# Performance work log

Hardware: AMD Instinct MI355X
Metric: run time of the kernel (lower is better)

The kernel has to match this reference:

```python
import jax, jax.numpy as jnp
import numpy as np
from jax import lax

N = 16384          # total nodes
NUM_GRAPHS = 256   # graphs in the batch
K = 50             # self.knn
NUM_BINS = 5       # num_edge_features
RDF_CUTOFF = 10.0  # Angstrom-scale cutoff for Gaussian RDF smearing
BIG = 1e10         # masked-distance sentinel (finite, jit-safe)


def setup_inputs() -> dict:
    key = jax.random.key(0)
    k1, k2 = jax.random.split(key)
    # 3D pharmacophore coordinates, ~Angstrom scale
    pos = jax.random.normal(k1, (N, 3), dtype=jnp.float32) * 3.0
    # sorted graph-id vector (PyG `batch`)
    batch = jnp.sort(jax.random.randint(k2, (N,), 0, NUM_GRAPHS, dtype=jnp.int64))
    return {"pos": pos, "batch": batch}


def reference(pos, batch):
    n = pos.shape[0]
    # --- brute-force KNN graph (T.KNNGraph, per-graph via batch mask) ---
    sq = jnp.sum(pos * pos, axis=-1)                         # [n]
    d2 = sq[:, None] + sq[None, :] - 2.0 * (pos @ pos.T)     # [n, n]
    same_graph = batch[:, None] == batch[None, :]
    valid = same_graph & ~jnp.eye(n, dtype=bool)             # no self-loops
    d2m = jnp.where(valid, d2, BIG)
    neg_d2, nbr_idx = lax.top_k(-d2m, K)                     # [n, K] nearest by distance
    # symmetric-superset edge list: j -> i (source_to_target flow)
    src = nbr_idx.reshape(-1)                                # [n*K]
    dst = jnp.repeat(jnp.arange(n), K)                       # [n*K]
    edge_index = jnp.stack([src, dst])                       # [2, n*K]
    # --- T.Distance(norm=False): raw Euclidean edge lengths ---
    dist = jnp.sqrt(jnp.maximum(-neg_d2, 1e-12)).reshape(-1)  # [n*K]
    # --- DistanceRDF(num_bins): Gaussian smearing of distances over bins ---
    centers = jnp.linspace(0.0, RDF_CUTOFF, NUM_BINS, dtype=pos.dtype)
    spacing = RDF_CUTOFF / (NUM_BINS - 1)
    gamma = 1.0 / (2.0 * spacing * spacing)
    rdf = jnp.exp(-gamma * (dist[:, None] - centers[None, :]) ** 2)  # [n*K, NUM_BINS]
    return edge_index, dist, rdf
```

## Files before the change

### kernel.cpp

```cpp
#include <hip/hip_runtime.h>
#include <math.h>

#define NTOT  16384
#define NGR   256
#define KNN   50
#define NBINS 5
#define BIGF  1e10f
#define MAXJ  3

__global__ void bounds_kernel(const int* __restrict__ batch, int* __restrict__ bounds)
{
    const int t = blockIdx.x * blockDim.x + threadIdx.x;
    if (t > NGR) return;
    int lo = 0, hi = NTOT;
    while (lo < hi) {
        const int mid = (lo + hi) >> 1;
        if (batch[mid] < t) lo = mid + 1; else hi = mid;
    }
    bounds[t] = lo;
}

__device__ __forceinline__ float bcast_lane(float v, int l)
{
    return __uint_as_float(__builtin_amdgcn_readlane(__float_as_uint(v), l));
}

template <int JJ>
__device__ __forceinline__ void rank_loop(const float (&d2r)[MAXJ], int (&rank)[MAXJ],
                                          int cnt, int lane)
{
    #pragma unroll
    for (int j2 = 0; j2 < JJ; ++j2) {
        const int base = j2 * 64;
        const int kmax = min(64, cnt - base);
        const float mine = d2r[j2];
        for (int l2 = 0; l2 < kmax; ++l2) {
            const float dk = bcast_lane(mine, l2);
            const int k = base + l2;
            #pragma unroll
            for (int j = 0; j < JJ; ++j) {
                const int c = j * 64 + lane;
                rank[j] += (dk < d2r[j]) || (dk == d2r[j] && k < c);
            }
        }
    }
}

__global__ __launch_bounds__(256)
void knn_main(const float* __restrict__ pos,
              const int*   __restrict__ batch,
              const int*   __restrict__ bounds,
              float*       __restrict__ out)
{
    const int wid  = (blockIdx.x << 2) + (threadIdx.x >> 6);
    const int lane = threadIdx.x & 63;
    const int i = wid;
    if (i >= NTOT) return;

    const int g     = batch[i];
    const int start = bounds[g];
    const int end   = bounds[g + 1];
    const int cnt   = end - start;
    const int J     = (cnt + 63) >> 6;

    const float xi = pos[(size_t)i * 3 + 0];
    const float yi = pos[(size_t)i * 3 + 1];
    const float zi = pos[(size_t)i * 3 + 2];
    const float sqi = xi * xi + yi * yi + zi * zi;

    float d2r[MAXJ];
    #pragma unroll
    for (int j = 0; j < MAXJ; ++j) d2r[j] = BIGF;

    #pragma unroll
    for (int j = 0; j < MAXJ; ++j) {
        const int c = j * 64 + lane;
        if (j < J && c < cnt) {
            const int idx = start + c;
            float d2 = BIGF;
            if (idx != i) {
                const float xj = pos[(size_t)idx * 3 + 0];
                const float yj = pos[(size_t)idx * 3 + 1];
                const float zj = pos[(size_t)idx * 3 + 2];
                const float sqj = xj * xj + yj * yj + zj * zj;
                const float dot = xi * xj + yi * yj + zi * zj;
                d2 = sqi + sqj - 2.0f * dot;
            }
            d2r[j] = d2;
        }
    }

    int rank[MAXJ] = {0, 0, 0};
    if      (J == 1) rank_loop<1>(d2r, rank, cnt, lane);
    else if (J == 2) rank_loop<2>(d2r, rank, cnt, lane);
    else             rank_loop<3>(d2r, rank, cnt, lane);

    float* __restrict__ srcO  = out;
    float* __restrict__ dstO  = out + (size_t)NTOT * KNN;
    float* __restrict__ distO = out + (size_t)2 * NTOT * KNN;
    float* __restrict__ rdfO  = out + (size_t)3 * NTOT * KNN;

    const float centers[NBINS] = {0.0f, 2.5f, 5.0f, 7.5f, 10.0f};
    const float gamma = 0.08f;
    const float fi = (float)i;

    #pragma unroll
    for (int j = 0; j < MAXJ; ++j) {
        const int c = j * 64 + lane;
        if (j < J && c < cnt && (start + c) != i) {
            const int r = rank[j];
            if (r < KNN) {
                const size_t e = (size_t)i * KNN + r;
                srcO[e]  = (float)(start + c);
                dstO[e]  = fi;
                const float d = sqrtf(fmaxf(d2r[j], 1e-12f));
                distO[e] = d;
                #pragma unroll
                for (int b = 0; b < NBINS; ++b) {
                    const float dd = d - centers[b];
                    rdfO[e * NBINS + b] = expf(-gamma * dd * dd);
                }
            }
        }
    }

    for (int r = (cnt - 1) + lane; r < KNN; r += 64) {
        const int m = r - (cnt - 1);
        int jj;
        if (m < start)       jj = m;
        else if (m == start) jj = i;
        else                 jj = end + (m - start - 1);
        const size_t e = (size_t)i * KNN + r;
        srcO[e]  = (float)jj;
        dstO[e]  = fi;
        const float d = sqrtf(BIGF);
        distO[e] = d;
        #pragma unroll
        for (int b = 0; b < NBINS; ++b) {
            const float dd = d - centers[b];
            rdfO[e * NBINS + b] = expf(-gamma * dd * dd);
        }
    }
}

extern "C" void kernel_launch(void* const* d_in, const int* in_sizes, int n_in,
                              void* d_out, int out_size, void* d_ws, size_t ws_size,
                              hipStream_t stream) {
    const float* pos   = (const float*)d_in[0];
    const int*   batch = (const int*)d_in[1];
    float*       out   = (float*)d_out;
    int*         bounds = (int*)d_ws;

    bounds_kernel<<<dim3(1), dim3(320), 0, stream>>>(batch, bounds);
    knn_main<<<dim3(NTOT / 4), dim3(256), 0, stream>>>(pos, batch, bounds, out);
}
```

Measured before the change: 90.68 us.

## Rank neighbors with packed 64-bit sortable keys and parallelize graph-bounds search

Packs each candidate's squared distance, transformed into an order-preserving integer, together with its index into one 64-bit key. Counting rank then needs a single unsigned compare per pair instead of a float compare plus tie-break, and the broadcast loop is unrolled by 8. The graph-bounds kernel now runs one thread per node and writes boundaries wherever the graph id changes, replacing a per-graph binary search. It also uses fast __expf, writes constant padding values for the underflowing far-distance case, and adds an occupancy hint. The key-transform edge cases and the hardcoded padding constants could affect exactness.

```diff
diff --git a/kernel.cpp b/kernel.cpp
--- a/kernel.cpp
+++ b/kernel.cpp
@@ -8,54 +8,53 @@
 #define BIGF  1e10f
 #define MAXJ  3
 
-__global__ void bounds_kernel(const int* __restrict__ batch, int* __restrict__ bounds)
+__global__ __launch_bounds__(256)
+void bounds_kernel(const int* __restrict__ batch, int* __restrict__ bounds)
 {
-    const int t = blockIdx.x * blockDim.x + threadIdx.x;
-    if (t > NGR) return;
-    int lo = 0, hi = NTOT;
-    while (lo < hi) {
-        const int mid = (lo + hi) >> 1;
-        if (batch[mid] < t) lo = mid + 1; else hi = mid;
-    }
-    bounds[t] = lo;
+    const int i = blockIdx.x * 256 + threadIdx.x;
+    if (i > NTOT) return;
+    const int cur  = (i < NTOT) ? batch[i] : NGR;
+    const int prev = (i == 0) ? -1 : batch[i - 1];
+    for (int t = prev + 1; t <= cur; ++t) bounds[t] = i;
 }
 
-__device__ __forceinline__ float bcast_lane(float v, int l)
+__device__ __forceinline__ unsigned int rdlane(unsigned int v, int l)
 {
-    return __uint_as_float(__builtin_amdgcn_readlane(__float_as_uint(v), l));
+    return (unsigned int)__builtin_amdgcn_readlane((int)v, l);
 }
 
-template <int JJ>
-__device__ __forceinline__ void rank_loop(const float (&d2r)[MAXJ], int (&rank)[MAXJ],
-                                          int cnt, int lane)
+template <int J>
+__device__ __forceinline__ void rank_count(const unsigned long long (&key)[MAXJ],
+                                           int (&rank)[MAXJ], int cnt)
 {
     #pragma unroll
-    for (int j2 = 0; j2 < JJ; ++j2) {
+    for (int j2 = 0; j2 < J; ++j2) {
         const int base = j2 * 64;
         const int kmax = min(64, cnt - base);
-        const float mine = d2r[j2];
-        for (int l2 = 0; l2 < kmax; ++l2) {
-            const float dk = bcast_lane(mine, l2);
-            const int k = base + l2;
+        const int kpad = (kmax + 7) & ~7;
+        const unsigned int mlo = (unsigned int)key[j2];
+        const unsigned int mhi = (unsigned int)(key[j2] >> 32);
+        for (int k0 = 0; k0 < kpad; k0 += 8) {
             #pragma unroll
-            for (int j = 0; j < JJ; ++j) {
-                const int c = j * 64 + lane;
-                rank[j] += (dk < d2r[j]) || (dk == d2r[j] && k < c);
+            for (int u = 0; u < 8; ++u) {
+                const unsigned int lo = rdlane(mlo, k0 + u);
+                const unsigned int hi = rdlane(mhi, k0 + u);
+                const unsigned long long kk = ((unsigned long long)hi << 32) | lo;
+                #pragma unroll
+                for (int j = 0; j < J; ++j) rank[j] += (kk < key[j]);
             }
         }
     }
 }
 
-__global__ __launch_bounds__(256)
+__global__ __launch_bounds__(256, 8)
 void knn_main(const float* __restrict__ pos,
               const int*   __restrict__ batch,
               const int*   __restrict__ bounds,
               float*       __restrict__ out)
 {
-    const int wid  = (blockIdx.x << 2) + (threadIdx.x >> 6);
+    const int i    = __builtin_amdgcn_readfirstlane((int)(blockIdx.x * 4 + (threadIdx.x >> 6)));
     const int lane = threadIdx.x & 63;
-    const int i = wid;
-    if (i >= NTOT) return;
 
     const int g     = batch[i];
     const int start = bounds[g];
@@ -68,32 +67,31 @@
     const float zi = pos[(size_t)i * 3 + 2];
     const float sqi = xi * xi + yi * yi + zi * zi;
 
-    float d2r[MAXJ];
-    #pragma unroll
-    for (int j = 0; j < MAXJ; ++j) d2r[j] = BIGF;
-
+    float d2s[MAXJ];
+    unsigned long long key[MAXJ];
     #pragma unroll
     for (int j = 0; j < MAXJ; ++j) {
         const int c = j * 64 + lane;
-        if (j < J && c < cnt) {
+        float d2 = BIGF;
+        if (j < J && c < cnt && (start + c) != i) {
             const int idx = start + c;
-            float d2 = BIGF;
-            if (idx != i) {
-                const float xj = pos[(size_t)idx * 3 + 0];
-                const float yj = pos[(size_t)idx * 3 + 1];
-                const float zj = pos[(size_t)idx * 3 + 2];
-                const float sqj = xj * xj + yj * yj + zj * zj;
-                const float dot = xi * xj + yi * yj + zi * zj;
-                d2 = sqi + sqj - 2.0f * dot;
-            }
-            d2r[j] = d2;
+            const float xj = pos[(size_t)idx * 3 + 0];
+            const float yj = pos[(size_t)idx * 3 + 1];
+            const float zj = pos[(size_t)idx * 3 + 2];
+            const float sqj = xj * xj + yj * yj + zj * zj;
+            const float dot = xi * xj + yi * yj + zi * zj;
+            d2 = sqi + sqj - 2.0f * dot;
         }
+        d2s[j] = d2;
+        const unsigned int b = __float_as_uint(d2);
+        const unsigned int s = ((int)b < 0) ? ~b : (b | 0x80000000u);
+        key[j] = ((unsigned long long)s << 32) | (unsigned int)(start + c);
     }
 
     int rank[MAXJ] = {0, 0, 0};
-    if      (J == 1) rank_loop<1>(d2r, rank, cnt, lane);
-    else if (J == 2) rank_loop<2>(d2r, rank, cnt, lane);
-    else             rank_loop<3>(d2r, rank, cnt, lane);
+    if      (J == 1) rank_count<1>(key, rank, cnt);
+    else if (J == 2) rank_count<2>(key, rank, cnt);
+    else             rank_count<3>(key, rank, cnt);
 
     float* __restrict__ srcO  = out;
     float* __restrict__ dstO  = out + (size_t)NTOT * KNN;
@@ -107,38 +105,35 @@
     #pragma unroll
     for (int j = 0; j < MAXJ; ++j) {
         const int c = j * 64 + lane;
-        if (j < J && c < cnt && (start + c) != i) {
-            const int r = rank[j];
-            if (r < KNN) {
-                const size_t e = (size_t)i * KNN + r;
-                srcO[e]  = (float)(start + c);
-                dstO[e]  = fi;
-                const float d = sqrtf(fmaxf(d2r[j], 1e-12f));
-                distO[e] = d;
-                #pragma unroll
-                for (int b = 0; b < NBINS; ++b) {
-                    const float dd = d - centers[b];
-                    rdfO[e * NBINS + b] = expf(-gamma * dd * dd);
-                }
+        if (j < J && c < cnt && (start + c) != i && rank[j] < KNN) {
+            const size_t e = (size_t)i * KNN + rank[j];
+            srcO[e]  = (float)(start + c);
+            dstO[e]  = fi;
+            const float d = sqrtf(fmaxf(d2s[j], 1e-12f));
+            distO[e] = d;
+            #pragma unroll
+            for (int b = 0; b < NBINS; ++b) {
+                const float dd = d - centers[b];
+                rdfO[e * NBINS + b] = __expf(-gamma * dd * dd);
             }
         }
     }
 
-    for (int r = (cnt - 1) + lane; r < KNN; r += 64) {
-        const int m = r - (cnt - 1);
-        int jj;
-        if (m < start)       jj = m;
-        else if (m == start) jj = i;
-        else                 jj = end + (m - start - 1);
-        const size_t e = (size_t)i * KNN + r;
-        srcO[e]  = (float)jj;
-        dstO[e]  = fi;
-        const float d = sqrtf(BIGF);
-        distO[e] = d;
-        #pragma unroll
-        for (int b = 0; b < NBINS; ++b) {
-            const float dd = d - centers[b];
-            rdfO[e * NBINS + b] = expf(-gamma * dd * dd);
+    if (cnt <= KNN) {
+        const int r = (cnt - 1) + lane;
+        if (r < KNN) {
+            const int m = lane;
+            int jj;
+            if (m < start)       jj = m;
+            else if (m == start) jj = i;
+            else                 jj = end + (m - start - 1);
+            const size_t e = (size_t)i * KNN + r;
+            srcO[e]  = (float)jj;
+            dstO[e]  = fi;
+            distO[e] = 100000.0f;
+            #pragma unroll
+            for (int b = 0; b < NBINS; ++b)
+                rdfO[e * NBINS + b] = 0.0f;
         }
     }
 }
@@ -146,11 +141,11 @@
 extern "C" void kernel_launch(void* const* d_in, const int* in_sizes, int n_in,
                               void* d_out, int out_size, void* d_ws, size_t ws_size,
                               hipStream_t stream) {
-    const float* pos   = (const float*)d_in[0];
-    const int*   batch = (const int*)d_in[1];
-    float*       out   = (float*)d_out;
+    const float* pos    = (const float*)d_in[0];
+    const int*   batch  = (const int*)d_in[1];
+    float*       out    = (float*)d_out;
     int*         bounds = (int*)d_ws;
 
-    bounds_kernel<<<dim3(1), dim3(320), 0, stream>>>(batch, bounds);
+    bounds_kernel<<<dim3(65), dim3(256), 0, stream>>>(batch, bounds);
     knn_main<<<dim3(NTOT / 4), dim3(256), 0, stream>>>(pos, batch, bounds, out);
 }
```

After: 83.30 us. 1.09x faster.
